# Kernel tuning notes

Measured on AMD Instinct MI355X. Metric: run time of the kernel, lower is better.

Reference implementation:

```python
import jax, jax.numpy as jnp
import numpy as np
from jax import lax

ALIGNED_H = 7
ALIGNED_W = 7
SPATIAL_SCALE = 0.125
B, C, H, W = 4, 512, 96, 96
R = 512
IMG = 768  # image resolution (features are image/8)


def setup_inputs() -> dict:
    key = jax.random.key(0)
    k1, k2, k3, k4, k5, k6 = jax.random.split(key, 6)
    features = jax.random.normal(k1, (B, C, H, W), dtype=jnp.float32)
    # realistic rois: [batch_idx, x1, y1, x2, y2] in image coordinates
    bi = jax.random.randint(k2, (R,), 0, B).astype(jnp.float32)
    cx = jax.random.uniform(k3, (R,), minval=32.0, maxval=float(IMG - 32))
    cy = jax.random.uniform(k4, (R,), minval=32.0, maxval=float(IMG - 32))
    bw = jax.random.uniform(k5, (R,), minval=16.0, maxval=256.0)
    bh = jax.random.uniform(k6, (R,), minval=16.0, maxval=256.0)
    x1 = jnp.clip(cx - bw / 2, 0.0, IMG - 1.0)
    x2 = jnp.clip(cx + bw / 2, 0.0, IMG - 1.0)
    y1 = jnp.clip(cy - bh / 2, 0.0, IMG - 1.0)
    y2 = jnp.clip(cy + bh / 2, 0.0, IMG - 1.0)
    rois = jnp.stack([bi, x1, y1, x2, y2], axis=1)
    return {"features": features, "rois": rois}


def _roi_align_ada(features, rois, ah, aw, scale):
    """RoIAlignAda: per output pixel, average of a 3x3 adaptive-stride grid of
    bilinear samples centered at the bin point (RT-MDNet ROIAlignAdaForward)."""
    b, c, h, w = features.shape
    r = rois.shape[0]
    batch_ind = rois[:, 0].astype(jnp.int32)
    x1 = rois[:, 1] * scale
    y1 = rois[:, 2] * scale
    x2 = rois[:, 3] * scale
    y2 = rois[:, 4] * scale
    roi_w = jnp.maximum(x2 - x1, 0.0)
    roi_h = jnp.maximum(y2 - y1, 0.0)
    bin_h = roi_h / (ah - 1.0)  # [R]
    bin_w = roi_w / (aw - 1.0)
    ph = jnp.arange(ah, dtype=jnp.float32)
    pw = jnp.arange(aw, dtype=jnp.float32)
    hc = y1[:, None] + ph[None, :] * bin_h[:, None]  # [R, AH] bin centers
    wc = x1[:, None] + pw[None, :] * bin_w[:, None]  # [R, AW]
    stride_h = jnp.maximum(1.0, jnp.round(bin_h / 3.0))  # [R]
    stride_w = jnp.maximum(1.0, jnp.round(bin_w / 3.0))

    center_ok = ((hc >= 0) & (hc < h))[:, :, None] & ((wc >= 0) & (wc < w))[:, None, :]  # [R,AH,AW]

    # flatten spatial for gathers: [B*H*W, C]
    f = features.transpose(0, 2, 3, 1).reshape(b * h * w, c)
    base = batch_ind[:, None, None] * (h * w)  # [R,1,1]

    acc = jnp.zeros((r, ah, aw, c), dtype=features.dtype)
    cnt = jnp.zeros((r, ah, aw), dtype=features.dtype)
    for sh in (-1.0, 0.0, 1.0):
        for sw in (-1.0, 0.0, 1.0):
            ch = hc + sh * stride_h[:, None]  # [R,AH]
            cw = wc + sw * stride_w[:, None]  # [R,AW]
            valid = ((ch >= 0) & (ch < h))[:, :, None] & ((cw >= 0) & (cw < w))[:, None, :]
            hs = jnp.clip(jnp.floor(ch), 0.0, h - 2.0)
            ws = jnp.clip(jnp.floor(cw), 0.0, w - 2.0)
            hr = (ch - hs)[:, :, None]  # [R,AH,1]
            wr = (cw - ws)[:, None, :] * jnp.ones((r, ah, aw), features.dtype)[:, :1, :1]  # broadcast helper
            wr = (cw - ws)[:, None, :]  # [R,1,AW]
            hsi = hs.astype(jnp.int32)[:, :, None]  # [R,AH,1]
            wsi = ws.astype(jnp.int32)[:, None, :]  # [R,1,AW]
            ul = base + hsi * w + wsi  # [R,AH,AW]
            v = (f[ul] * ((1.0 - hr) * (1.0 - wr))[..., None]
                 + f[ul + 1] * ((1.0 - hr) * wr)[..., None]
                 + f[ul + w] * (hr * (1.0 - wr))[..., None]
                 + f[ul + w + 1] * (hr * wr)[..., None])  # [R,AH,AW,C]
            acc = acc + jnp.where(valid[..., None], v, 0.0)
            cnt = cnt + valid.astype(features.dtype)

    out = jnp.where(center_ok[..., None], acc / jnp.maximum(cnt, 1.0)[..., None], 0.0)
    return out.transpose(0, 3, 1, 2)  # [R, C, AH, AW]


def reference(features, rois):
    x = _roi_align_ada(features, rois, ALIGNED_H + 4, ALIGNED_W + 4, SPATIAL_SCALE)  # [R,C,11,11]
    # fused 3x3 stride-2 max pool -> [R, C, 5, 5]
    out = lax.reduce_window(x, -jnp.inf, lax.max,
                            window_dimensions=(1, 1, 3, 3),
                            window_strides=(1, 1, 2, 2),
                            padding='VALID')
    return out
```

## Files before the change

kernel.cpp:

```cpp
#include <hip/hip_runtime.h>
#include <stdint.h>

typedef unsigned short u16;
typedef unsigned int   u32;

#define Bn 4
#define Cc 512
#define Hh 96
#define Ww 96
#define HWc (Hh*Ww)
#define AH 11
#define Rr 512
#define CP (Cc/2)

__device__ __forceinline__ u16 f2bf(float f){
  u32 u = __float_as_uint(f);
  u += 0x7fffu + ((u>>16)&1u);
  return (u16)(u>>16);
}

__global__ __launch_bounds__(256)
void transpose_kernel(const float* __restrict__ in, u32* __restrict__ out){
  __shared__ u16 tile[64][66];
  const int t = threadIdx.x;
  const int hw0 = blockIdx.x*64, c0 = blockIdx.y*64, b = blockIdx.z;
  {
    const int hwq = (t & 15)*4, cl0 = t >> 4;
    const float* ib = in + ((size_t)(b*Cc + c0))*HWc + hw0;
    #pragma unroll
    for (int p=0;p<4;++p){
      int cl = cl0 + p*16;
      float4 v = *(const float4*)(ib + (size_t)cl*HWc + hwq);
      tile[cl][hwq+0] = f2bf(v.x);
      tile[cl][hwq+1] = f2bf(v.y);
      tile[cl][hwq+2] = f2bf(v.z);
      tile[cl][hwq+3] = f2bf(v.w);
    }
  }
  __syncthreads();
  {
    const int cp = t & 31, hwb = t >> 5;
    u32* ob = out + ((size_t)b*HWc + hw0)*CP + (c0>>1);
    #pragma unroll
    for (int p=0;p<8;++p){
      int hw = hwb + p*8;
      u32 lo = tile[2*cp  ][hw];
      u32 hi = tile[2*cp+1][hw];
      ob[(size_t)hw*CP + cp] = lo | (hi<<16);
    }
  }
}


template<int LO, int NPH, int NOY>
__device__ __forceinline__ void roi_seg_body(
    const u32* __restrict__ fb,
    const int   (*s_roff4)[4], const float (*s_rw4)[4],
    const int   (*s_coff4)[4], const float (*s_cw4)[4],
    float* __restrict__ s_out, int t)
{
  float2 awin[5];
  #pragma unroll 1
  for (int lp=0; lp<NPH; ++lp){
    const int ph = LO + lp;
    const int4   ro4 = *(const int4*)  s_roff4[ph];
    const float4 rw4 = *(const float4*)s_rw4[ph];
    const int   ro_[4] = {ro4.x, ro4.y, ro4.z, ro4.w};
    const float rw_[4] = {rw4.x, rw4.y, rw4.z, rw4.w};
    float2 binr[AH];
    #pragma unroll
    for (int pw=0; pw<AH; ++pw){
      const int4   co4 = *(const int4*)  s_coff4[pw];
      const float4 cw4 = *(const float4*)s_cw4[pw];
      const int   co_[4] = {co4.x, co4.y, co4.z, co4.w};
      const float cw_[4] = {cw4.x, cw4.y, cw4.z, cw4.w};
      u32 v[16];
      #pragma unroll
      for (int i=0;i<4;++i)
        #pragma unroll
        for (int j=0;j<4;++j)
          v[i*4+j] = fb[ro_[i] + co_[j]];
      float ax=0.0f, ay=0.0f;
      #pragma unroll
      for (int i=0;i<4;++i)
        #pragma unroll
        for (int j=0;j<4;++j){
          float w = rw_[i]*cw_[j];
          u32 d = v[i*4+j];
          ax = fmaf(w, __uint_as_float(d<<16),           ax);
          ay = fmaf(w, __uint_as_float(d & 0xffff0000u), ay);
        }
      binr[pw] = make_float2(ax, ay);
    }
    float2 rm[5];
    #pragma unroll
    for (int ox=0; ox<5; ++ox){
      rm[ox].x = fmaxf(fmaxf(binr[2*ox].x, binr[2*ox+1].x), binr[2*ox+2].x);
      rm[ox].y = fmaxf(fmaxf(binr[2*ox].y, binr[2*ox+1].y), binr[2*ox+2].y);
    }
    if (lp == 0){
      #pragma unroll
      for (int ox=0; ox<5; ++ox) awin[ox] = rm[ox];
    } else if (lp & 1){
      #pragma unroll
      for (int ox=0; ox<5; ++ox){
        awin[ox].x = fmaxf(awin[ox].x, rm[ox].x);
        awin[ox].y = fmaxf(awin[ox].y, rm[ox].y);
      }
    } else {
      const int ol = (lp-2) >> 1;
      #pragma unroll
      for (int ox=0; ox<5; ++ox){
        s_out[(2*t  )*(NOY*5) + ol*5 + ox] = fmaxf(awin[ox].x, rm[ox].x);
        s_out[(2*t+1)*(NOY*5) + ol*5 + ox] = fmaxf(awin[ox].y, rm[ox].y);
        awin[ox] = rm[ox];
      }
    }
  }
}

__global__ __launch_bounds__(256)
void roi_align_max_nhwc(const u32* __restrict__ feat,
                        const float* __restrict__ rois,
                        float* __restrict__ out)
{
  __shared__ __align__(16) int   s_roff4[AH][4];
  __shared__ __align__(16) float s_rw4  [AH][4];
  __shared__ __align__(16) int   s_coff4[AH][4];
  __shared__ __align__(16) float s_cw4  [AH][4];
  __shared__ int s_b;
  __shared__ __align__(16) float s_out[Cc*15];

  const int t   = threadIdx.x;
  const int r   = blockIdx.x >> 1;
  const int seg = blockIdx.x & 1;

  if (t == 0){
    int b = (int)rois[r*5+0];
    s_b = min(max(b, 0), Bn-1);
  }

  if (t < AH || (t >= 64 && t < 64+AH)){
    const bool isrow = (t < AH);
    const int  p = isrow ? t : t-64;
    const float* rp = rois + r*5;
    const float c1 = rp[isrow?2:1], c2 = rp[isrow?4:3];
    float lo  = __fmul_rn(c1, 0.125f);
    float hi  = __fmul_rn(c2, 0.125f);
    float ext = fmaxf(__fsub_rn(hi,lo), 0.0f);
    float bin = __fdiv_rn(ext, 10.0f);
    float ctr = __fadd_rn(lo, __fmul_rn((float)p, bin));
    float strd = fmaxf(1.0f, rintf(__fdiv_rn(bin, 3.0f)));
    bool ok = (ctr >= 0.0f) && (ctr < 96.0f);
    int rws[6]; float wts[6]; int nv=0;
    #pragma unroll
    for (int s=0;s<3;++s){
      float cc = __fadd_rn(ctr, __fmul_rn((float)(s-1), strd));
      bool vv = (cc >= 0.0f) && (cc < 96.0f);
      float fl = fminf(fmaxf(floorf(cc),0.0f),94.0f);
      float fr = __fsub_rn(cc, fl);
      int ri = (int)fl;
      rws[2*s]=ri; rws[2*s+1]=ri+1;
      wts[2*s]  = vv ? __fsub_rn(1.0f,fr) : 0.0f;
      wts[2*s+1]= vv ? fr : 0.0f;
      nv += vv?1:0;
    }
    float sc = ok ? (1.0f/(float)nv) : 0.0f;
    int cr[4]={0,0,0,0}; float cwv[4]={0.0f,0.0f,0.0f,0.0f}; int n=0;
    for (int k=0;k<6;++k){
      float wk=wts[k]; if (wk==0.0f) continue;
      int rr=rws[k]; bool fnd=false;
      for (int j=0;j<n;++j) if (cr[j]==rr){ cwv[j]+=wk; fnd=true; break; }
      if (!fnd && n<4){ cr[n]=rr; cwv[n]=wk; ++n; }
    }
    const int mul = isrow ? (Ww*CP) : CP;
    #pragma unroll
    for (int k=0;k<4;++k){
      int off = cr[k]*mul;
      float wv = cwv[k]*sc;
      if (isrow){ s_roff4[p][k]=off; s_rw4[p][k]=wv; }
      else      { s_coff4[p][k]=off; s_cw4[p][k]=wv; }
    }
  }
  __syncthreads();

  const u32* fb = feat + (size_t)s_b*((size_t)HWc*CP) + t;

  if (seg == 0) roi_seg_body<0,5,2>(fb, s_roff4, s_rw4, s_coff4, s_cw4, s_out, t);
  else          roi_seg_body<4,7,3>(fb, s_roff4, s_rw4, s_coff4, s_cw4, s_out, t);
  __syncthreads();

  if (seg == 0){
    float* dst = out + (size_t)r*(Cc*25);
    for (int k=t; k<Cc*10; k+=256){
      int c = k/10, j = k - c*10;
      dst[c*25 + j] = s_out[k];
    }
  } else {
    float* dst = out + (size_t)r*(Cc*25) + 10;
    for (int k=t; k<Cc*15; k+=256){
      int c = k/15, j = k - c*15;
      dst[c*25 + j] = s_out[k];
    }
  }
}

__global__ __launch_bounds__(512, 1)
void roi_align_max_nchw(const float* __restrict__ feat,
                        const float* __restrict__ rois,
                        float* __restrict__ out)
{
  __shared__ int   s_roff[AH][6];
  __shared__ float s_rw  [AH][6];
  __shared__ int   s_coff[AH][6];
  __shared__ float s_cw  [AH][6];
  __shared__ int   s_b;
  __shared__ __align__(16) float s_out[Cc*25];

  const int t = threadIdx.x;
  const int r = blockIdx.x;

  if (t < AH*6){
    ((float*)s_rw)[t] = 0.0f;  ((int*)s_roff)[t] = 0;
    ((float*)s_cw)[t] = 0.0f;  ((int*)s_coff)[t] = 0;
  }
  if (t == 0){
    int b = (int)rois[r*5+0];
    s_b = min(max(b, 0), Bn-1);
  }
  __syncthreads();

  if (t < AH || (t >= 64 && t < 64+AH)){
    const bool isrow = (t < AH);
    const int  p = isrow ? t : t-64;
    const float* rp = rois + r*5;
    const float c1 = rp[isrow?2:1], c2 = rp[isrow?4:3];
    float lo  = __fmul_rn(c1, 0.125f);
    float hi  = __fmul_rn(c2, 0.125f);
    float ext = fmaxf(__fsub_rn(hi,lo), 0.0f);
    float bin = __fdiv_rn(ext, 10.0f);
    float ctr = __fadd_rn(lo, __fmul_rn((float)p, bin));
    float strd = fmaxf(1.0f, rintf(__fdiv_rn(bin, 3.0f)));
    bool ok = (ctr >= 0.0f) && (ctr < 96.0f);
    int rws[6]; float wts[6]; int nv=0;
    #pragma unroll
    for (int s=0;s<3;++s){
      float cc = __fadd_rn(ctr, __fmul_rn((float)(s-1), strd));
      bool vv = (cc >= 0.0f) && (cc < 96.0f);
      float fl = fminf(fmaxf(floorf(cc),0.0f),94.0f);
      float fr = __fsub_rn(cc, fl);
      int ri = (int)fl;
      rws[2*s]=ri; rws[2*s+1]=ri+1;
      wts[2*s]  = vv ? __fsub_rn(1.0f,fr) : 0.0f;
      wts[2*s+1]= vv ? fr : 0.0f;
      nv += vv?1:0;
    }
    float sc = ok ? (1.0f/(float)nv) : 0.0f;
    int cr[6]; float cw[6]; int n=0;
    for (int k=0;k<6;++k){
      float wk=wts[k]; if (wk==0.0f) continue;
      if (n>0 && cr[n-1]==rws[k]) cw[n-1]+=wk;
      else { cr[n]=rws[k]; cw[n]=wk; ++n; }
    }
    const int mul = isrow ? Ww : 1;
    for (int k=0;k<n;++k){
      int off = cr[k]*mul;
      float wv = cw[k]*sc;
      if (isrow){ s_roff[p][k]=off; s_rw[p][k]=wv; }
      else      { s_coff[p][k]=off; s_cw[p][k]=wv; }
    }
  }
  __syncthreads();

  const float* f0 = feat + ((size_t)s_b*Cc + t)*HWc;
  float awin[5];
  for (int ph=0; ph<AH; ++ph){
    float binrow[AH];
    #pragma unroll
    for (int pw=0; pw<AH; ++pw){
      float acc = 0.0f;
      #pragma unroll
      for (int ai=0; ai<6; ++ai){
        float ra = s_rw[ph][ai];
        if (ra == 0.0f) continue;
        int ro = s_roff[ph][ai];
        #pragma unroll
        for (int bi=0; bi<6; ++bi){
          float cb = s_cw[pw][bi];
          if (cb == 0.0f) continue;
          acc = fmaf(ra*cb, f0[ro + s_coff[pw][bi]], acc);
        }
      }
      binrow[pw] = acc;
    }
    float rm[5];
    #pragma unroll
    for (int ox=0; ox<5; ++ox)
      rm[ox] = fmaxf(fmaxf(binrow[2*ox], binrow[2*ox+1]), binrow[2*ox+2]);
    if (ph == 0){
      #pragma unroll
      for (int ox=0; ox<5; ++ox) awin[ox] = rm[ox];
    } else if (ph & 1){
      #pragma unroll
      for (int ox=0; ox<5; ++ox) awin[ox] = fmaxf(awin[ox], rm[ox]);
    } else {
      int oy = (ph-2) >> 1;
      #pragma unroll
      for (int ox=0; ox<5; ++ox){
        s_out[t*25 + oy*5 + ox] = fmaxf(awin[ox], rm[ox]);
        awin[ox] = rm[ox];
      }
    }
  }
  __syncthreads();

  float4* dst = (float4*)(out + (size_t)r*(Cc*25));
  const float4* src = (const float4*)s_out;
  for (int k=t; k<(Cc*25)/4; k+=512) dst[k]=src[k];
}

extern "C" void kernel_launch(void* const* d_in, const int* in_sizes, int n_in,
                              void* d_out, int out_size, void* d_ws, size_t ws_size,
                              hipStream_t stream)
{
  (void)in_sizes; (void)n_in; (void)out_size;
  const float* feat = (const float*)d_in[0];
  const float* rois = (const float*)d_in[1];
  float* out = (float*)d_out;
  const size_t need = (size_t)Bn*HWc*Cc*sizeof(u16);
  if (ws_size >= need){
    u32* ws = (u32*)d_ws;
    dim3 g(HWc/64, Cc/64, Bn);
    transpose_kernel<<<g, 256, 0, stream>>>(feat, ws);
    roi_align_max_nhwc<<<Rr*2, 256, 0, stream>>>(ws, rois, out);
  } else {
    roi_align_max_nchw<<<Rr, 512, 0, stream>>>(feat, rois, out);
  }
}
```

Before: 196.1 us.

## Split ROI work by channel halves and enlarge bf16 transpose tiles

The ROI kernel now gives each block half of the channels for all 11 rows, using 128 threads, instead of splitting by output rows with redundant overlapping rows. That removes the duplicated row computation and allows a contiguous float4 output store. It also precomputes per-thread column offsets in registers and makes the row base pointers scalar via readfirstlane. The transpose packs channel pairs while reading and uses 128x128 tiles with coalesced 64-lane row writes. The tradeoffs are fewer threads per block and higher register pressure from the precomputed offset arrays.

After: 176.9 us. 1.11x faster.

```diff
diff --git a/kernel.cpp b/kernel.cpp
--- a/kernel.cpp
+++ b/kernel.cpp
@@ -21,119 +21,52 @@
 
 __global__ __launch_bounds__(256)
 void transpose_kernel(const float* __restrict__ in, u32* __restrict__ out){
-  __shared__ u16 tile[64][66];
+  __shared__ u32 tile[128][65];
   const int t = threadIdx.x;
-  const int hw0 = blockIdx.x*64, c0 = blockIdx.y*64, b = blockIdx.z;
+  const int hw0 = blockIdx.x*128, c0 = blockIdx.y*128, b = blockIdx.z;
   {
-    const int hwq = (t & 15)*4, cl0 = t >> 4;
-    const float* ib = in + ((size_t)(b*Cc + c0))*HWc + hw0;
-    #pragma unroll
-    for (int p=0;p<4;++p){
-      int cl = cl0 + p*16;
-      float4 v = *(const float4*)(ib + (size_t)cl*HWc + hwq);
-      tile[cl][hwq+0] = f2bf(v.x);
-      tile[cl][hwq+1] = f2bf(v.y);
-      tile[cl][hwq+2] = f2bf(v.z);
-      tile[cl][hwq+3] = f2bf(v.w);
+    const int q   = t & 31;
+    const int cp0 = t >> 5;
+    const float* ib = in + ((size_t)(b*Cc + c0))*HWc + hw0 + 4*q;
+    #pragma unroll
+    for (int p=0;p<8;++p){
+      const int cp = cp0 + p*8;
+      const float* pa = ib + (size_t)(2*cp)*HWc;
+      float4 A = *(const float4*)pa;
+      float4 B = *(const float4*)(pa + HWc);
+      tile[4*q+0][cp] = (u32)f2bf(A.x) | ((u32)f2bf(B.x)<<16);
+      tile[4*q+1][cp] = (u32)f2bf(A.y) | ((u32)f2bf(B.y)<<16);
+      tile[4*q+2][cp] = (u32)f2bf(A.z) | ((u32)f2bf(B.z)<<16);
+      tile[4*q+3][cp] = (u32)f2bf(A.w) | ((u32)f2bf(B.w)<<16);
     }
   }
   __syncthreads();
   {
-    const int cp = t & 31, hwb = t >> 5;
-    u32* ob = out + ((size_t)b*HWc + hw0)*CP + (c0>>1);
-    #pragma unroll
-    for (int p=0;p<8;++p){
-      int hw = hwb + p*8;
-      u32 lo = tile[2*cp  ][hw];
-      u32 hi = tile[2*cp+1][hw];
-      ob[(size_t)hw*CP + cp] = lo | (hi<<16);
-    }
-  }
-}
-
-
-template<int LO, int NPH, int NOY>
-__device__ __forceinline__ void roi_seg_body(
-    const u32* __restrict__ fb,
-    const int   (*s_roff4)[4], const float (*s_rw4)[4],
-    const int   (*s_coff4)[4], const float (*s_cw4)[4],
-    float* __restrict__ s_out, int t)
-{
-  float2 awin[5];
-  #pragma unroll 1
-  for (int lp=0; lp<NPH; ++lp){
-    const int ph = LO + lp;
-    const int4   ro4 = *(const int4*)  s_roff4[ph];
-    const float4 rw4 = *(const float4*)s_rw4[ph];
-    const int   ro_[4] = {ro4.x, ro4.y, ro4.z, ro4.w};
-    const float rw_[4] = {rw4.x, rw4.y, rw4.z, rw4.w};
-    float2 binr[AH];
-    #pragma unroll
-    for (int pw=0; pw<AH; ++pw){
-      const int4   co4 = *(const int4*)  s_coff4[pw];
-      const float4 cw4 = *(const float4*)s_cw4[pw];
-      const int   co_[4] = {co4.x, co4.y, co4.z, co4.w};
-      const float cw_[4] = {cw4.x, cw4.y, cw4.z, cw4.w};
-      u32 v[16];
-      #pragma unroll
-      for (int i=0;i<4;++i)
-        #pragma unroll
-        for (int j=0;j<4;++j)
-          v[i*4+j] = fb[ro_[i] + co_[j]];
-      float ax=0.0f, ay=0.0f;
-      #pragma unroll
-      for (int i=0;i<4;++i)
-        #pragma unroll
-        for (int j=0;j<4;++j){
-          float w = rw_[i]*cw_[j];
-          u32 d = v[i*4+j];
-          ax = fmaf(w, __uint_as_float(d<<16),           ax);
-          ay = fmaf(w, __uint_as_float(d & 0xffff0000u), ay);
-        }
-      binr[pw] = make_float2(ax, ay);
-    }
-    float2 rm[5];
-    #pragma unroll
-    for (int ox=0; ox<5; ++ox){
-      rm[ox].x = fmaxf(fmaxf(binr[2*ox].x, binr[2*ox+1].x), binr[2*ox+2].x);
-      rm[ox].y = fmaxf(fmaxf(binr[2*ox].y, binr[2*ox+1].y), binr[2*ox+2].y);
-    }
-    if (lp == 0){
-      #pragma unroll
-      for (int ox=0; ox<5; ++ox) awin[ox] = rm[ox];
-    } else if (lp & 1){
-      #pragma unroll
-      for (int ox=0; ox<5; ++ox){
-        awin[ox].x = fmaxf(awin[ox].x, rm[ox].x);
-        awin[ox].y = fmaxf(awin[ox].y, rm[ox].y);
-      }
-    } else {
-      const int ol = (lp-2) >> 1;
-      #pragma unroll
-      for (int ox=0; ox<5; ++ox){
-        s_out[(2*t  )*(NOY*5) + ol*5 + ox] = fmaxf(awin[ox].x, rm[ox].x);
-        s_out[(2*t+1)*(NOY*5) + ol*5 + ox] = fmaxf(awin[ox].y, rm[ox].y);
-        awin[ox] = rm[ox];
-      }
-    }
-  }
-}
-
-__global__ __launch_bounds__(256)
+    const int l = t & 63, wv = t >> 6;
+    u32* ob = out + ((size_t)b*HWc + hw0)*CP + (c0>>1) + l;
+    #pragma unroll
+    for (int k=0;k<32;++k){
+      const int hw = wv*32 + k;
+      ob[(size_t)hw*CP] = tile[hw][l];
+    }
+  }
+}
+
+__global__ __launch_bounds__(128)
 void roi_align_max_nhwc(const u32* __restrict__ feat,
                         const float* __restrict__ rois,
                         float* __restrict__ out)
 {
-  __shared__ __align__(16) int   s_roff4[AH][4];
-  __shared__ __align__(16) float s_rw4  [AH][4];
-  __shared__ __align__(16) int   s_coff4[AH][4];
-  __shared__ __align__(16) float s_cw4  [AH][4];
+  __shared__ __align__(16) int4   s_ro[AH];
+  __shared__ __align__(16) float4 s_rw[AH];
+  __shared__ __align__(16) int4   s_co[AH];
+  __shared__ __align__(16) float4 s_cw[AH];
   __shared__ int s_b;
-  __shared__ __align__(16) float s_out[Cc*15];
-
-  const int t   = threadIdx.x;
-  const int r   = blockIdx.x >> 1;
-  const int seg = blockIdx.x & 1;
+  __shared__ __align__(16) float s_out[256*25];
+
+  const int t    = threadIdx.x;
+  const int r    = blockIdx.x >> 1;
+  const int half = blockIdx.x & 1;
 
   if (t == 0){
     int b = (int)rois[r*5+0];
@@ -174,35 +107,90 @@
       if (!fnd && n<4){ cr[n]=rr; cwv[n]=wk; ++n; }
     }
     const int mul = isrow ? (Ww*CP) : CP;
-    #pragma unroll
-    for (int k=0;k<4;++k){
-      int off = cr[k]*mul;
-      float wv = cwv[k]*sc;
-      if (isrow){ s_roff4[p][k]=off; s_rw4[p][k]=wv; }
-      else      { s_coff4[p][k]=off; s_cw4[p][k]=wv; }
-    }
-  }
-  __syncthreads();
-
-  const u32* fb = feat + (size_t)s_b*((size_t)HWc*CP) + t;
-
-  if (seg == 0) roi_seg_body<0,5,2>(fb, s_roff4, s_rw4, s_coff4, s_cw4, s_out, t);
-  else          roi_seg_body<4,7,3>(fb, s_roff4, s_rw4, s_coff4, s_cw4, s_out, t);
-  __syncthreads();
-
-  if (seg == 0){
-    float* dst = out + (size_t)r*(Cc*25);
-    for (int k=t; k<Cc*10; k+=256){
-      int c = k/10, j = k - c*10;
-      dst[c*25 + j] = s_out[k];
-    }
-  } else {
-    float* dst = out + (size_t)r*(Cc*25) + 10;
-    for (int k=t; k<Cc*15; k+=256){
-      int c = k/15, j = k - c*15;
-      dst[c*25 + j] = s_out[k];
-    }
-  }
+    if (isrow){
+      s_ro[p] = make_int4(cr[0]*mul, cr[1]*mul, cr[2]*mul, cr[3]*mul);
+      s_rw[p] = make_float4(cwv[0]*sc, cwv[1]*sc, cwv[2]*sc, cwv[3]*sc);
+    } else {
+      s_co[p] = make_int4(cr[0]*mul, cr[1]*mul, cr[2]*mul, cr[3]*mul);
+      s_cw[p] = make_float4(cwv[0]*sc, cwv[1]*sc, cwv[2]*sc, cwv[3]*sc);
+    }
+  }
+  __syncthreads();
+
+  const u32* fbase = feat + (size_t)s_b*((size_t)HWc*CP);
+  const int tb = half*128 + t;
+
+  int   vo[AH][4]; float cwr[AH][4];
+  #pragma unroll
+  for (int pw=0; pw<AH; ++pw){
+    int4 c4 = s_co[pw]; float4 w4 = s_cw[pw];
+    vo[pw][0]=tb+c4.x; vo[pw][1]=tb+c4.y; vo[pw][2]=tb+c4.z; vo[pw][3]=tb+c4.w;
+    cwr[pw][0]=w4.x; cwr[pw][1]=w4.y; cwr[pw][2]=w4.z; cwr[pw][3]=w4.w;
+  }
+
+  float2 awin[5];
+  #pragma unroll 1
+  for (int ph=0; ph<AH; ++ph){
+    int4   r4 = s_ro[ph];
+    float4 w4 = s_rw[ph];
+    const u32* r0 = fbase + __builtin_amdgcn_readfirstlane(r4.x);
+    const u32* r1 = fbase + __builtin_amdgcn_readfirstlane(r4.y);
+    const u32* r2 = fbase + __builtin_amdgcn_readfirstlane(r4.z);
+    const u32* r3 = fbase + __builtin_amdgcn_readfirstlane(r4.w);
+    const float rw_[4] = {w4.x, w4.y, w4.z, w4.w};
+    float2 binr[AH];
+    #pragma unroll
+    for (int pw=0; pw<AH; ++pw){
+      u32 v[16];
+      #pragma unroll
+      for (int j=0;j<4;++j){
+        v[0*4+j] = r0[vo[pw][j]];
+        v[1*4+j] = r1[vo[pw][j]];
+        v[2*4+j] = r2[vo[pw][j]];
+        v[3*4+j] = r3[vo[pw][j]];
+      }
+      float ax=0.0f, ay=0.0f;
+      #pragma unroll
+      for (int i=0;i<4;++i)
+        #pragma unroll
+        for (int j=0;j<4;++j){
+          float w = rw_[i]*cwr[pw][j];
+          u32 d = v[i*4+j];
+          ax = fmaf(w, __uint_as_float(d<<16),           ax);
+          ay = fmaf(w, __uint_as_float(d & 0xffff0000u), ay);
+        }
+      binr[pw] = make_float2(ax, ay);
+    }
+    float2 rm[5];
+    #pragma unroll
+    for (int ox=0; ox<5; ++ox){
+      rm[ox].x = fmaxf(fmaxf(binr[2*ox].x, binr[2*ox+1].x), binr[2*ox+2].x);
+      rm[ox].y = fmaxf(fmaxf(binr[2*ox].y, binr[2*ox+1].y), binr[2*ox+2].y);
+    }
+    if (ph == 0){
+      #pragma unroll
+      for (int ox=0; ox<5; ++ox) awin[ox] = rm[ox];
+    } else if (ph & 1){
+      #pragma unroll
+      for (int ox=0; ox<5; ++ox){
+        awin[ox].x = fmaxf(awin[ox].x, rm[ox].x);
+        awin[ox].y = fmaxf(awin[ox].y, rm[ox].y);
+      }
+    } else {
+      const int oy = (ph-2) >> 1;
+      #pragma unroll
+      for (int ox=0; ox<5; ++ox){
+        s_out[(2*t  )*25 + oy*5 + ox] = fmaxf(awin[ox].x, rm[ox].x);
+        s_out[(2*t+1)*25 + oy*5 + ox] = fmaxf(awin[ox].y, rm[ox].y);
+        awin[ox] = rm[ox];
+      }
+    }
+  }
+  __syncthreads();
+
+  float4* dst = (float4*)(out + (size_t)r*(Cc*25) + half*(256*25));
+  const float4* src = (const float4*)s_out;
+  for (int k=t; k<(256*25)/4; k+=128) dst[k]=src[k];
 }
 
 __global__ __launch_bounds__(512, 1)
@@ -330,9 +318,9 @@
   const size_t need = (size_t)Bn*HWc*Cc*sizeof(u16);
   if (ws_size >= need){
     u32* ws = (u32*)d_ws;
-    dim3 g(HWc/64, Cc/64, Bn);
+    dim3 g(HWc/128, Cc/128, Bn);
     transpose_kernel<<<g, 256, 0, stream>>>(feat, ws);
-    roi_align_max_nhwc<<<Rr*2, 256, 0, stream>>>(ws, rois, out);
+    roi_align_max_nhwc<<<Rr*2, 128, 0, stream>>>(ws, rois, out);
   } else {
     roi_align_max_nchw<<<Rr, 512, 0, stream>>>(feat, rois, out);
   }
```
